# Performance work log

Measured on AMD Instinct MI355X. Metric: run time of the kernel, lower is better.

The kernel has to match this reference:

```python
import jax, jax.numpy as jnp
import numpy as np

A2B = 1.8897259886          # angstrom -> bohr
EV2HA = 0.0367493
NUM_RBF = 16
R_MIN = 0.5 * A2B
R_MAX = 4.0 * A2B           # r_max_angstroms=4.0 from gnn_config
RBF_WIDTH = (R_MAX - R_MIN) / NUM_RBF
N_NODES = 100_000
N_EDGES = 3_200_000
EMBED_DIM = 16
N_ELEMS = 4
CODES_PER_ELEM = 4          # all elements are core -> max_codes_per_element
TOTAL_CODES = N_ELEMS * CODES_PER_ELEM
NUM_PAIRS = 10
CODE_OWNER = np.repeat(np.arange(N_ELEMS), CODES_PER_ELEM)  # element owning each code


def setup_inputs() -> dict:
    key = jax.random.key(0)
    ks = jax.random.split(key, 12)
    N, E, D = N_NODES, N_EDGES, EMBED_DIM
    inv_sp = lambda v: np.float32(np.log(np.expm1(v)))  # inverse_softplus
    return {
        "elem_idx": jax.random.randint(ks[0], (N,), 0, N_ELEMS),
        "edge_index": jax.random.randint(ks[1], (2, E), 0, N),
        "distances": jax.random.uniform(ks[2], (E,), minval=1.0, maxval=7.5),  # bohr
        "pair_idx": jax.random.randint(ks[3], (E,), 0, NUM_PAIRS),
        "embed": jax.random.normal(ks[4], (N_ELEMS, D)),
        "fw1": jax.random.normal(ks[5], (D, NUM_RBF)) * 0.3,
        "fb1": jnp.zeros((D,)),
        "fw2": jax.random.normal(ks[6], (D, D)) * 0.3,
        "fb2": jnp.zeros((D,)),
        "mw1": jax.random.normal(ks[7], (D, D)) * 0.3,
        "mb1": jnp.zeros((D,)),
        "mw2": jax.random.normal(ks[8], (3, D)) * 0.05,  # zero-init in orig; small random for a live baseline
        "mb2": jnp.zeros((3,)),
        "codebook": jax.random.normal(ks[9], (TOTAL_CODES, D)),
        "raw_D_e": jnp.full((NUM_PAIRS,), inv_sp(0.1 * EV2HA)),
        "raw_alpha": jnp.full((NUM_PAIRS,), inv_sp(1.5 / A2B)),
        "raw_r0": jnp.full((NUM_PAIRS,), np.float32(3.0 * A2B)),
    }


def reference(elem_idx, edge_index, distances, pair_idx, embed,
              fw1, fb1, fw2, fb2, mw1, mb1, mw2, mb2,
              codebook, raw_D_e, raw_alpha, raw_r0):
    # --- EnvironmentEncoder: gather + edge filter + scatter_add ---
    h = embed[elem_idx]                                              # [N, D]
    centers = jnp.linspace(R_MIN, R_MAX, NUM_RBF, dtype=distances.dtype)
    rbf = jnp.exp(-0.5 * ((distances[:, None] - centers) / RBF_WIDTH) ** 2)  # [E, RBF]
    W = jax.nn.silu(rbf @ fw1.T + fb1) @ fw2.T + fb2                 # [E, D]
    src, tgt = edge_index[0], edge_index[1]
    messages = h[tgt] * W                                            # [E, D]
    agg = jax.ops.segment_sum(messages, src, num_segments=h.shape[0])
    h = h + agg                                                      # [N, D]

    # --- VectorQuantizer (eval path): per-element masked cdist + argmin ---
    d2 = (jnp.sum(h * h, axis=1, keepdims=True)
          - 2.0 * h @ codebook.T
          + jnp.sum(codebook * codebook, axis=1))                    # [N, C] squared dist
    owner = jnp.asarray(CODE_OWNER)
    valid = elem_idx[:, None] == owner[None, :]                      # [N, C]
    atom_types = jnp.argmin(jnp.where(valid, d2, jnp.inf), axis=1)   # [N]
    z_q = codebook[atom_types]                                       # [N, D]
    h_q = h + jax.lax.stop_gradient(z_q - h)                         # straight-through
    # all elements have >1 code -> commitment over all atoms
    vq_loss = 0.25 * jnp.mean((h - jax.lax.stop_gradient(z_q)) ** 2)

    # --- MorseParameterPredictor: edge gather + MLP ---
    pair_feat = h_q[src] + h_q[tgt]                                  # [E, D]
    delta = jax.nn.silu(pair_feat @ mw1.T + mb1) @ mw2.T + mb2       # [E, 3]

    D_e = jax.nn.softplus(raw_D_e[pair_idx] + delta[:, 0])
    alpha = jax.nn.softplus(raw_alpha[pair_idx] + delta[:, 1])
    r0 = raw_r0[pair_idx] + delta[:, 2]
    params = jnp.stack([D_e, alpha, r0], axis=-1)                    # [E, 3]
    return params, vq_loss
```

## Files before the change

kernel.cpp:

```cpp
#include <hip/hip_runtime.h>
#include <stdint.h>

#define A2B   1.8897259886f
#define R_MIN (0.5f * A2B)
#define R_MAX (4.0f * A2B)

#define EPB 2048

__global__ void __launch_bounds__(256) k_bucket(
        const int* __restrict__ src, const int* __restrict__ tgt,
        const int* __restrict__ elem, const float* __restrict__ dist,
        int* __restrict__ gCursor, float* __restrict__ dBuf,
        unsigned short* __restrict__ kBuf, int CAP, int SHIFT, int E)
{
    __shared__ int cnt[256], base_[256];
    int t = threadIdx.x;
    cnt[t] = 0;
    __syncthreads();
    int e0 = blockIdx.x * EPB;
    int eEnd = (e0 + EPB < E) ? e0 + EPB : E;

    float dv[8]; int bv[8]; unsigned short kv[8];
    #pragma unroll
    for (int j = 0; j < 8; ++j) {
        int e = e0 + t + j * 256;
        if (e < eEnd) {
            int s = src[e];
            int q = elem[tgt[e]];
            dv[j] = dist[e];
            int b = s >> SHIFT;
            bv[j] = b;
            kv[j] = (unsigned short)(((s - (b << SHIFT)) << 2) | q);
            atomicAdd(&cnt[b], 1);
        }
    }
    __syncthreads();
    if (cnt[t] > 0) base_[t] = atomicAdd(&gCursor[t], cnt[t]);
    __syncthreads();
    cnt[t] = 0;
    __syncthreads();
    #pragma unroll
    for (int j = 0; j < 8; ++j) {
        int e = e0 + t + j * 256;
        if (e < eEnd) {
            int b = bv[j];
            int pos = base_[b] + atomicAdd(&cnt[b], 1);
            if (pos < CAP) {
                size_t idx = (size_t)b * CAP + pos;
                dBuf[idx] = dv[j];
                kBuf[idx] = kv[j];
            }
        }
    }
}

__global__ void __launch_bounds__(256) k_bscan(
        const int* __restrict__ gCursor, int* __restrict__ bucketBase,
        int* __restrict__ offs4, int NBUK, int N4, int E)
{
    __shared__ int sd[256];
    int t = threadIdx.x;
    int v = (t < NBUK) ? gCursor[t] : 0;
    sd[t] = v; __syncthreads();
    #pragma unroll
    for (int o = 1; o < 256; o <<= 1) {
        int x = (t >= o) ? sd[t - o] : 0;
        __syncthreads();
        sd[t] += x;
        __syncthreads();
    }
    bucketBase[t] = sd[t] - v;
    if (t == 0) offs4[N4] = E;
}

__global__ void __launch_bounds__(256) k_bin(
        const float* __restrict__ dBuf, const unsigned short* __restrict__ kBuf,
        const int* __restrict__ gCursor, const int* __restrict__ bucketBase,
        int* __restrict__ offs4, float* __restrict__ payload,
        int CAP, int SHIFT, int N)
{
    __shared__ int lcnt[2048];
    __shared__ int sd[256];
    int t = threadIdx.x, b = blockIdx.x;
    int n0 = b << SHIFT;
    int n1 = n0 + (1 << SHIFT); if (n1 > N) n1 = N;
    int m  = (n1 - n0) * 4;
    int cntE = gCursor[b]; if (cntE > CAP) cntE = CAP;
    int base = bucketBase[b];
    for (int i = t; i < m; i += 256) lcnt[i] = 0;
    __syncthreads();
    const float* dB = dBuf + (size_t)b * CAP;
    const unsigned short* kB = kBuf + (size_t)b * CAP;
    for (int i = t; i < cntE; i += 256)
        atomicAdd(&lcnt[kB[i]], 1);
    __syncthreads();
    int v[8]; int tsum = 0; int b8 = t * 8;
    #pragma unroll
    for (int j = 0; j < 8; ++j) { v[j] = (b8 + j < m) ? lcnt[b8 + j] : 0; tsum += v[j]; }
    sd[t] = tsum; __syncthreads();
    #pragma unroll
    for (int o = 1; o < 256; o <<= 1) {
        int x = (t >= o) ? sd[t - o] : 0;
        __syncthreads();
        sd[t] += x;
        __syncthreads();
    }
    int run = sd[t] - tsum;
    #pragma unroll
    for (int j = 0; j < 8; ++j) {
        if (b8 + j < m) {
            int c = v[j];
            lcnt[b8 + j] = run;
            offs4[n0 * 4 + b8 + j] = base + run;
            run += c;
        }
    }
    __syncthreads();
    for (int i = t; i < cntE; i += 256) {
        int pos = atomicAdd(&lcnt[kB[i]], 1);
        payload[base + pos] = dB[i];
    }
}

__global__ void __launch_bounds__(256) k_gather(
        const int* __restrict__ elem, const float* __restrict__ embed,
        const float* __restrict__ codebook,
        const float* __restrict__ fw1, const float* __restrict__ fb1,
        const float* __restrict__ fw2, const float* __restrict__ fb2,
        const int* __restrict__ offs4, const float* __restrict__ payload,
        int* __restrict__ atype, float* __restrict__ loss, int N)
{
    __shared__ float4 s_fw1t[64];
    __shared__ float4 s_fw2v[64];
    __shared__ float s_cb[256];
    __shared__ float s_fb1[16], s_fb2[16], s_emb[64], s_cbn[16];
    __shared__ float s_red[4];
    int t = threadIdx.x;
    {
        float* f1 = (float*)s_fw1t;
        f1[(t & 15) * 16 + (t >> 4)] = fw1[t];
        float* f2 = (float*)s_fw2v;
        f2[t] = fw2[t];
        s_cb[t] = codebook[t];
    }
    if (t < 16) { s_fb1[t] = fb1[t]; s_fb2[t] = fb2[t]; }
    if (t < 64) s_emb[t] = embed[t];
    __syncthreads();
    if (t < 16) {
        float s = 0.f;
        #pragma unroll
        for (int j = 0; j < 16; ++j) { float c = s_cb[t * 16 + j]; s += c * c; }
        s_cbn[t] = s;
    }
    __syncthreads();

    int node = blockIdx.x * 32 + (t >> 3);
    int sub  = t & 7;
    float lp = 0.0f;
    float acc[16];
    #pragma unroll
    for (int j = 0; j < 16; ++j) acc[j] = 0.f;

    if (node < N) {
        const float invw   = 16.0f / (R_MAX - R_MIN);
        const float u0base = R_MIN * invw;
        const float kstep  = 16.0f / 15.0f;
        #pragma clang loop unroll(disable)
        for (int qq = 0; qq < 4; ++qq) {
            int b0 = offs4[node * 4 + qq], b1 = offs4[node * 4 + qq + 1];
            if (b0 == b1) continue;
            float G[16];
            #pragma unroll
            for (int j = 0; j < 16; ++j) G[j] = 0.f;
            for (int i = b0 + sub; i < b1; i += 16) {
                int ii = i + 8;
                bool has2 = (ii < b1);
                float d0 = payload[i];
                float d1 = has2 ? payload[ii] : d0;
                float ua = d0 * invw - u0base;
                float ub = d1 * invw - u0base;
                float g0[16], g1[16];
                #pragma unroll
                for (int i2 = 0; i2 < 16; ++i2) { g0[i2] = s_fb1[i2]; g1[i2] = s_fb1[i2]; }
                #pragma clang loop unroll(disable)
                for (int k = 0; k < 16; ++k) {
                    float r0 = __expf(-0.5f * ua * ua);
                    float r1 = __expf(-0.5f * ub * ub);
                    float4 w0 = s_fw1t[k*4+0], w1 = s_fw1t[k*4+1];
                    float4 w2 = s_fw1t[k*4+2], w3 = s_fw1t[k*4+3];
                    g0[0]+=r0*w0.x;  g0[1]+=r0*w0.y;  g0[2]+=r0*w0.z;  g0[3]+=r0*w0.w;
                    g0[4]+=r0*w1.x;  g0[5]+=r0*w1.y;  g0[6]+=r0*w1.z;  g0[7]+=r0*w1.w;
                    g0[8]+=r0*w2.x;  g0[9]+=r0*w2.y;  g0[10]+=r0*w2.z; g0[11]+=r0*w2.w;
                    g0[12]+=r0*w3.x; g0[13]+=r0*w3.y; g0[14]+=r0*w3.z; g0[15]+=r0*w3.w;
                    g1[0]+=r1*w0.x;  g1[1]+=r1*w0.y;  g1[2]+=r1*w0.z;  g1[3]+=r1*w0.w;
                    g1[4]+=r1*w1.x;  g1[5]+=r1*w1.y;  g1[6]+=r1*w1.z;  g1[7]+=r1*w1.w;
                    g1[8]+=r1*w2.x;  g1[9]+=r1*w2.y;  g1[10]+=r1*w2.z; g1[11]+=r1*w2.w;
                    g1[12]+=r1*w3.x; g1[13]+=r1*w3.y; g1[14]+=r1*w3.z; g1[15]+=r1*w3.w;
                    ua -= kstep; ub -= kstep;
                }
                #pragma unroll
                for (int i2 = 0; i2 < 16; ++i2) {
                    float a = g0[i2];
                    G[i2] += a * __builtin_amdgcn_rcpf(1.0f + __expf(-a));
                }
                if (has2) {
                    #pragma unroll
                    for (int i2 = 0; i2 < 16; ++i2) {
                        float a = g1[i2];
                        G[i2] += a * __builtin_amdgcn_rcpf(1.0f + __expf(-a));
                    }
                }
            }
            const float* er = s_emb + qq * 16;
            #pragma clang loop unroll_count(4)
            for (int j = 0; j < 16; ++j) {
                float4 f0 = s_fw2v[j*4+0], f1 = s_fw2v[j*4+1];
                float4 f2 = s_fw2v[j*4+2], f3 = s_fw2v[j*4+3];
                float w = G[0]*f0.x  + G[1]*f0.y  + G[2]*f0.z  + G[3]*f0.w
                        + G[4]*f1.x  + G[5]*f1.y  + G[6]*f1.z  + G[7]*f1.w
                        + G[8]*f2.x  + G[9]*f2.y  + G[10]*f2.z + G[11]*f2.w
                        + G[12]*f3.x + G[13]*f3.y + G[14]*f3.z + G[15]*f3.w;
                acc[j] += w * er[j];
            }
            if (sub == 0) {
                float nb = (float)(b1 - b0);
                #pragma unroll
                for (int j = 0; j < 16; ++j)
                    acc[j] += nb * s_fb2[j] * er[j];
            }
        }
        #pragma unroll
        for (int m = 1; m <= 4; m <<= 1) {
            #pragma unroll
            for (int j = 0; j < 16; ++j)
                acc[j] += __shfl_xor(acc[j], m, 64);
        }
        int qn = elem[node];
        float h[16], hh = 0.f;
        #pragma unroll
        for (int j = 0; j < 16; ++j) {
            h[j] = acc[j] + s_emb[qn * 16 + j];
            hh += h[j] * h[j];
        }
        float best = __builtin_inff(); int bi = 0;
        #pragma unroll
        for (int c = 0; c < 4; ++c) {
            int code = qn * 4 + c;
            float dot = 0.f;
            #pragma unroll
            for (int j = 0; j < 16; ++j) dot += h[j] * s_cb[code * 16 + j];
            float d2 = hh - 2.0f * dot + s_cbn[code];
            if (d2 < best) { best = d2; bi = code; }
        }
        if (sub == 0) {
            atype[node] = bi;
            #pragma unroll
            for (int j = 0; j < 16; ++j) {
                float df = h[j] - s_cb[bi * 16 + j];
                lp += df * df;
            }
        }
    }
    #pragma unroll
    for (int o = 32; o > 0; o >>= 1) lp += __shfl_down(lp, o, 64);
    int wid = t >> 6;
    if ((t & 63) == 0) s_red[wid] = lp;
    __syncthreads();
    if (t == 0) atomicAdd(loss, s_red[0] + s_red[1] + s_red[2] + s_red[3]);
}

__global__ void __launch_bounds__(256) k_table(
        const float* __restrict__ codebook,
        const float* __restrict__ mw1, const float* __restrict__ mb1,
        const float* __restrict__ mw2, const float* __restrict__ mb2,
        const float* __restrict__ rD, const float* __restrict__ rA,
        const float* __restrict__ rR,
        const float* __restrict__ loss, float4* __restrict__ table,
        float* __restrict__ out_loss, float inv_nd)
{
    __shared__ float s_cb[256], s_mw1[256], s_mb1[16], s_mw2[48], s_mb2[3];
    __shared__ float s_rd[10], s_ra[10], s_rr[10];
    int tid = threadIdx.x;
    s_cb[tid] = codebook[tid];
    s_mw1[tid] = mw1[tid];
    if (tid < 16) s_mb1[tid] = mb1[tid];
    if (tid < 48) s_mw2[tid] = mw2[tid];
    if (tid < 3)  s_mb2[tid] = mb2[tid];
    if (tid < 10) { s_rd[tid] = rD[tid]; s_ra[tid] = rA[tid]; s_rr[tid] = rR[tid]; }
    __syncthreads();

    int a = tid >> 4, b = tid & 15;
    float pf[16];
    #pragma unroll
    for (int j = 0; j < 16; ++j) pf[j] = s_cb[a * 16 + j] + s_cb[b * 16 + j];
    float hid[16];
    #pragma unroll
    for (int i = 0; i < 16; ++i) {
        float acc = s_mb1[i];
        #pragma unroll
        for (int j = 0; j < 16; ++j) acc += pf[j] * s_mw1[i * 16 + j];
        hid[i] = acc / (1.0f + __expf(-acc));
    }
    float del[3];
    #pragma unroll
    for (int r = 0; r < 3; ++r) {
        float acc = s_mb2[r];
        #pragma unroll
        for (int i = 0; i < 16; ++i) acc += hid[i] * s_mw2[r * 16 + i];
        del[r] = acc;
    }
    #pragma unroll
    for (int p = 0; p < 10; ++p) {
        float xd = s_rd[p] + del[0];
        float xa = s_ra[p] + del[1];
        float De = (xd > 20.f) ? xd : log1pf(__expf(xd));
        float al = (xa > 20.f) ? xa : log1pf(__expf(xa));
        float r0 = s_rr[p] + del[2];
        table[tid * 10 + p] = make_float4(De, al, r0, 0.f);
    }
    if (tid == 0) out_loss[0] = 0.25f * loss[0] * inv_nd;
}

__global__ void __launch_bounds__(256) k_out(
        const int* __restrict__ src, const int* __restrict__ tgt,
        const int* __restrict__ pidx, const int* __restrict__ atype,
        const float4* __restrict__ table, float2* __restrict__ out, int Ehalf)
{
    int i = blockIdx.x * 256 + threadIdx.x;
    if (i >= Ehalf) return;
    int2 s2 = ((const int2*)src)[i];
    int2 t2 = ((const int2*)tgt)[i];
    int2 p2 = ((const int2*)pidx)[i];
    int i0 = (atype[s2.x] * 16 + atype[t2.x]) * 10 + p2.x;
    int i1 = (atype[s2.y] * 16 + atype[t2.y]) * 10 + p2.y;
    float4 t0 = table[i0];
    float4 t1 = table[i1];
    float2* op = out + (size_t)3 * i;
    op[0] = make_float2(t0.x, t0.y);
    op[1] = make_float2(t0.z, t1.x);
    op[2] = make_float2(t1.y, t1.z);
}

extern "C" void kernel_launch(void* const* d_in, const int* in_sizes, int n_in,
                              void* d_out, int out_size, void* d_ws, size_t ws_size,
                              hipStream_t stream)
{
    (void)n_in;
    const int*   elem  = (const int*)d_in[0];
    const int*   eidx  = (const int*)d_in[1];
    const float* dist  = (const float*)d_in[2];
    const int*   pidx  = (const int*)d_in[3];
    const float* embed = (const float*)d_in[4];
    const float* fw1   = (const float*)d_in[5];
    const float* fb1   = (const float*)d_in[6];
    const float* fw2   = (const float*)d_in[7];
    const float* fb2   = (const float*)d_in[8];
    const float* mw1   = (const float*)d_in[9];
    const float* mb1   = (const float*)d_in[10];
    const float* mw2   = (const float*)d_in[11];
    const float* mb2   = (const float*)d_in[12];
    const float* cb    = (const float*)d_in[13];
    const float* rD    = (const float*)d_in[14];
    const float* rA    = (const float*)d_in[15];
    const float* rR    = (const float*)d_in[16];

    int N = in_sizes[0];
    int E = in_sizes[2];
    const int* src = eidx;
    const int* tgt = eidx + E;
    int N4 = N * 4;

    int SHIFT = 0;
    while ((1 << SHIFT) < (N + 255) / 256) SHIFT++;
    int NBUK = (N + (1 << SHIFT) - 1) >> SHIFT;
    long long expv = ((long long)E << SHIFT) / N;
    int CAP = (int)(expv + expv / 16 + 256);

    size_t outBytes = (size_t)out_size * 4;
    char* ob = (char*)d_out;
    size_t oc = 0;
    float* dBuf = (float*)(ob + oc);           oc += (size_t)NBUK * CAP * 4;
    unsigned short* kBuf = (unsigned short*)(ob + oc); oc += (size_t)NBUK * CAP * 2;
    oc = (oc + 3) & ~(size_t)3;
    float* payload = (float*)(ob + oc);        oc += (size_t)E * 4;
    int*   offs4   = (int*)(ob + oc);          oc += (size_t)(N4 + 1) * 4;
    if (oc > outBytes) return;

    char* ws = (char*)d_ws;
    size_t cur = 0;
    int*   gCursor    = (int*)(ws + cur);  cur += 256 * 4;
    float* loss       = (float*)(ws + cur); cur += 4;
    size_t clearB = cur;
    int*   bucketBase = (int*)(ws + cur);  cur += 256 * 4;
    int*   atype      = (int*)(ws + cur);  cur += (size_t)N * 4;
    cur = (cur + 15) & ~(size_t)15;
    float4* table     = (float4*)(ws + cur); cur += 2560 * sizeof(float4);
    if (ws_size < cur) return;

    hipMemsetAsync(d_ws, 0, clearB, stream);

    k_bucket<<<(E + EPB - 1) / EPB, 256, 0, stream>>>(
        src, tgt, elem, dist, gCursor, dBuf, kBuf, CAP, SHIFT, E);
    k_bscan<<<1, 256, 0, stream>>>(gCursor, bucketBase, offs4, NBUK, N4, E);
    k_bin<<<NBUK, 256, 0, stream>>>(dBuf, kBuf, gCursor, bucketBase,
                                    offs4, payload, CAP, SHIFT, N);
    k_gather<<<(N + 31) / 32, 256, 0, stream>>>(elem, embed, cb, fw1, fb1,
                                                fw2, fb2, offs4, payload,
                                                atype, loss, N);
    float* outl = (float*)d_out + (size_t)3 * E;
    k_table<<<1, 256, 0, stream>>>(cb, mw1, mb1, mw2, mb2, rD, rA, rR,
                                   loss, table, outl,
                                   1.0f / (float)((size_t)N * 16));
    k_out<<<(E / 2 + 255) / 256, 256, 0, stream>>>(src, tgt, pidx, atype, table,
                                                   (float2*)d_out, E / 2);
}
```

Baseline: 302.4 us.

## Bin edges per node only and pack source element into distance low bits

```diff
diff --git a/kernel.cpp b/kernel.cpp
--- a/kernel.cpp
+++ b/kernel.cpp
@@ -56,7 +56,7 @@
 
 __global__ void __launch_bounds__(256) k_bscan(
         const int* __restrict__ gCursor, int* __restrict__ bucketBase,
-        int* __restrict__ offs4, int NBUK, int N4, int E)
+        int* __restrict__ offs, int NBUK, int N, int E)
 {
     __shared__ int sd[256];
     int t = threadIdx.x;
@@ -70,21 +70,21 @@
         __syncthreads();
     }
     bucketBase[t] = sd[t] - v;
-    if (t == 0) offs4[N4] = E;
+    if (t == 0) offs[N] = E;
 }
 
 __global__ void __launch_bounds__(256) k_bin(
         const float* __restrict__ dBuf, const unsigned short* __restrict__ kBuf,
         const int* __restrict__ gCursor, const int* __restrict__ bucketBase,
-        int* __restrict__ offs4, float* __restrict__ payload,
+        int* __restrict__ offs, float* __restrict__ payload,
         int CAP, int SHIFT, int N)
 {
-    __shared__ int lcnt[2048];
+    __shared__ int lcnt[512];
     __shared__ int sd[256];
     int t = threadIdx.x, b = blockIdx.x;
     int n0 = b << SHIFT;
     int n1 = n0 + (1 << SHIFT); if (n1 > N) n1 = N;
-    int m  = (n1 - n0) * 4;
+    int m  = n1 - n0;
     int cntE = gCursor[b]; if (cntE > CAP) cntE = CAP;
     int base = bucketBase[b];
     for (int i = t; i < m; i += 256) lcnt[i] = 0;
@@ -92,11 +92,12 @@
     const float* dB = dBuf + (size_t)b * CAP;
     const unsigned short* kB = kBuf + (size_t)b * CAP;
     for (int i = t; i < cntE; i += 256)
-        atomicAdd(&lcnt[kB[i]], 1);
-    __syncthreads();
-    int v[8]; int tsum = 0; int b8 = t * 8;
-    #pragma unroll
-    for (int j = 0; j < 8; ++j) { v[j] = (b8 + j < m) ? lcnt[b8 + j] : 0; tsum += v[j]; }
+        atomicAdd(&lcnt[kB[i] >> 2], 1);
+    __syncthreads();
+    int b2 = t * 2;
+    int v0 = (b2 < m)     ? lcnt[b2]     : 0;
+    int v1 = (b2 + 1 < m) ? lcnt[b2 + 1] : 0;
+    int tsum = v0 + v1;
     sd[t] = tsum; __syncthreads();
     #pragma unroll
     for (int o = 1; o < 256; o <<= 1) {
@@ -106,19 +107,14 @@
         __syncthreads();
     }
     int run = sd[t] - tsum;
-    #pragma unroll
-    for (int j = 0; j < 8; ++j) {
-        if (b8 + j < m) {
-            int c = v[j];
-            lcnt[b8 + j] = run;
-            offs4[n0 * 4 + b8 + j] = base + run;
-            run += c;
-        }
-    }
+    if (b2 < m)     { lcnt[b2] = run;     offs[n0 + b2] = base + run;     run += v0; }
+    if (b2 + 1 < m) { lcnt[b2 + 1] = run; offs[n0 + b2 + 1] = base + run; run += v1; }
     __syncthreads();
     for (int i = t; i < cntE; i += 256) {
-        int pos = atomicAdd(&lcnt[kB[i]], 1);
-        payload[base + pos] = dB[i];
+        int kv = kB[i];
+        int pos = atomicAdd(&lcnt[kv >> 2], 1);
+        unsigned db = __float_as_uint(dB[i]);
+        payload[base + pos] = __uint_as_float((db & ~3u) | (unsigned)(kv & 3));
     }
 }
 
@@ -127,7 +123,7 @@
         const float* __restrict__ codebook,
         const float* __restrict__ fw1, const float* __restrict__ fb1,
         const float* __restrict__ fw2, const float* __restrict__ fb2,
-        const int* __restrict__ offs4, const float* __restrict__ payload,
+        const int* __restrict__ offs, const float* __restrict__ payload,
         int* __restrict__ atype, float* __restrict__ loss, int N)
 {
     __shared__ float4 s_fw1t[64];
@@ -154,86 +150,107 @@
     }
     __syncthreads();
 
-    int node = blockIdx.x * 32 + (t >> 3);
-    int sub  = t & 7;
+    int node = blockIdx.x * 64 + (t >> 2);
+    int sub  = t & 3;
     float lp = 0.0f;
-    float acc[16];
-    #pragma unroll
-    for (int j = 0; j < 16; ++j) acc[j] = 0.f;
-
     if (node < N) {
+        int o0 = offs[node], o1 = offs[node + 1];
+        float G0[16], G1[16], G2[16], G3[16];
+        #pragma unroll
+        for (int j = 0; j < 16; ++j) { G0[j]=0.f; G1[j]=0.f; G2[j]=0.f; G3[j]=0.f; }
+        float c0 = 0.f, c1 = 0.f, c2 = 0.f, c3 = 0.f;
+
         const float invw   = 16.0f / (R_MAX - R_MIN);
         const float u0base = R_MIN * invw;
         const float kstep  = 16.0f / 15.0f;
-        #pragma clang loop unroll(disable)
-        for (int qq = 0; qq < 4; ++qq) {
-            int b0 = offs4[node * 4 + qq], b1 = offs4[node * 4 + qq + 1];
-            if (b0 == b1) continue;
-            float G[16];
+        for (int i = o0 + sub; i < o1; i += 8) {
+            int ii = i + 4;
+            bool has2 = (ii < o1);
+            unsigned p0 = __float_as_uint(payload[i]);
+            unsigned p1 = has2 ? __float_as_uint(payload[ii]) : p0;
+            int q0 = (int)(p0 & 3u), q1 = (int)(p1 & 3u);
+            float d0 = __uint_as_float(p0 & ~3u);
+            float d1 = __uint_as_float(p1 & ~3u);
+            float ua = d0 * invw - u0base;
+            float ub = d1 * invw - u0base;
+            float g0[16], g1[16];
             #pragma unroll
-            for (int j = 0; j < 16; ++j) G[j] = 0.f;
-            for (int i = b0 + sub; i < b1; i += 16) {
-                int ii = i + 8;
-                bool has2 = (ii < b1);
-                float d0 = payload[i];
-                float d1 = has2 ? payload[ii] : d0;
-                float ua = d0 * invw - u0base;
-                float ub = d1 * invw - u0base;
-                float g0[16], g1[16];
-                #pragma unroll
-                for (int i2 = 0; i2 < 16; ++i2) { g0[i2] = s_fb1[i2]; g1[i2] = s_fb1[i2]; }
-                #pragma clang loop unroll(disable)
-                for (int k = 0; k < 16; ++k) {
-                    float r0 = __expf(-0.5f * ua * ua);
-                    float r1 = __expf(-0.5f * ub * ub);
-                    float4 w0 = s_fw1t[k*4+0], w1 = s_fw1t[k*4+1];
-                    float4 w2 = s_fw1t[k*4+2], w3 = s_fw1t[k*4+3];
-                    g0[0]+=r0*w0.x;  g0[1]+=r0*w0.y;  g0[2]+=r0*w0.z;  g0[3]+=r0*w0.w;
-                    g0[4]+=r0*w1.x;  g0[5]+=r0*w1.y;  g0[6]+=r0*w1.z;  g0[7]+=r0*w1.w;
-                    g0[8]+=r0*w2.x;  g0[9]+=r0*w2.y;  g0[10]+=r0*w2.z; g0[11]+=r0*w2.w;
-                    g0[12]+=r0*w3.x; g0[13]+=r0*w3.y; g0[14]+=r0*w3.z; g0[15]+=r0*w3.w;
-                    g1[0]+=r1*w0.x;  g1[1]+=r1*w0.y;  g1[2]+=r1*w0.z;  g1[3]+=r1*w0.w;
-                    g1[4]+=r1*w1.x;  g1[5]+=r1*w1.y;  g1[6]+=r1*w1.z;  g1[7]+=r1*w1.w;
-                    g1[8]+=r1*w2.x;  g1[9]+=r1*w2.y;  g1[10]+=r1*w2.z; g1[11]+=r1*w2.w;
-                    g1[12]+=r1*w3.x; g1[13]+=r1*w3.y; g1[14]+=r1*w3.z; g1[15]+=r1*w3.w;
-                    ua -= kstep; ub -= kstep;
-                }
+            for (int i2 = 0; i2 < 16; ++i2) { g0[i2] = s_fb1[i2]; g1[i2] = s_fb1[i2]; }
+            #pragma clang loop unroll(disable)
+            for (int k = 0; k < 16; ++k) {
+                float r0 = __expf(-0.5f * ua * ua);
+                float r1 = __expf(-0.5f * ub * ub);
+                float4 w0 = s_fw1t[k*4+0], w1 = s_fw1t[k*4+1];
+                float4 w2 = s_fw1t[k*4+2], w3 = s_fw1t[k*4+3];
+                g0[0]+=r0*w0.x;  g0[1]+=r0*w0.y;  g0[2]+=r0*w0.z;  g0[3]+=r0*w0.w;
+                g0[4]+=r0*w1.x;  g0[5]+=r0*w1.y;  g0[6]+=r0*w1.z;  g0[7]+=r0*w1.w;
+                g0[8]+=r0*w2.x;  g0[9]+=r0*w2.y;  g0[10]+=r0*w2.z; g0[11]+=r0*w2.w;
+                g0[12]+=r0*w3.x; g0[13]+=r0*w3.y; g0[14]+=r0*w3.z; g0[15]+=r0*w3.w;
+                g1[0]+=r1*w0.x;  g1[1]+=r1*w0.y;  g1[2]+=r1*w0.z;  g1[3]+=r1*w0.w;
+                g1[4]+=r1*w1.x;  g1[5]+=r1*w1.y;  g1[6]+=r1*w1.z;  g1[7]+=r1*w1.w;
+                g1[8]+=r1*w2.x;  g1[9]+=r1*w2.y;  g1[10]+=r1*w2.z; g1[11]+=r1*w2.w;
+                g1[12]+=r1*w3.x; g1[13]+=r1*w3.y; g1[14]+=r1*w3.z; g1[15]+=r1*w3.w;
+                ua -= kstep; ub -= kstep;
+            }
+            {
+                float m0 = (q0==0)?1.f:0.f, m1 = (q0==1)?1.f:0.f;
+                float m2 = (q0==2)?1.f:0.f, m3 = (q0==3)?1.f:0.f;
+                c0 += m0; c1 += m1; c2 += m2; c3 += m3;
                 #pragma unroll
                 for (int i2 = 0; i2 < 16; ++i2) {
                     float a = g0[i2];
-                    G[i2] += a * __builtin_amdgcn_rcpf(1.0f + __expf(-a));
+                    float s = a * __builtin_amdgcn_rcpf(1.0f + __expf(-a));
+                    G0[i2] += m0*s; G1[i2] += m1*s; G2[i2] += m2*s; G3[i2] += m3*s;
                 }
-                if (has2) {
-                    #pragma unroll
-                    for (int i2 = 0; i2 < 16; ++i2) {
-                        float a = g1[i2];
-                        G[i2] += a * __builtin_amdgcn_rcpf(1.0f + __expf(-a));
-                    }
+            }
+            if (has2) {
+                float m0 = (q1==0)?1.f:0.f, m1 = (q1==1)?1.f:0.f;
+                float m2 = (q1==2)?1.f:0.f, m3 = (q1==3)?1.f:0.f;
+                c0 += m0; c1 += m1; c2 += m2; c3 += m3;
+                #pragma unroll
+                for (int i2 = 0; i2 < 16; ++i2) {
+                    float a = g1[i2];
+                    float s = a * __builtin_amdgcn_rcpf(1.0f + __expf(-a));
+                    G0[i2] += m0*s; G1[i2] += m1*s; G2[i2] += m2*s; G3[i2] += m3*s;
                 }
             }
-            const float* er = s_emb + qq * 16;
-            #pragma clang loop unroll_count(4)
+        }
+        #pragma unroll
+        for (int mm = 1; mm <= 2; mm <<= 1) {
+            #pragma unroll
             for (int j = 0; j < 16; ++j) {
-                float4 f0 = s_fw2v[j*4+0], f1 = s_fw2v[j*4+1];
-                float4 f2 = s_fw2v[j*4+2], f3 = s_fw2v[j*4+3];
-                float w = G[0]*f0.x  + G[1]*f0.y  + G[2]*f0.z  + G[3]*f0.w
-                        + G[4]*f1.x  + G[5]*f1.y  + G[6]*f1.z  + G[7]*f1.w
-                        + G[8]*f2.x  + G[9]*f2.y  + G[10]*f2.z + G[11]*f2.w
-                        + G[12]*f3.x + G[13]*f3.y + G[14]*f3.z + G[15]*f3.w;
-                acc[j] += w * er[j];
-            }
-            if (sub == 0) {
-                float nb = (float)(b1 - b0);
-                #pragma unroll
-                for (int j = 0; j < 16; ++j)
-                    acc[j] += nb * s_fb2[j] * er[j];
-            }
-        }
-        #pragma unroll
-        for (int m = 1; m <= 4; m <<= 1) {
+                G0[j] += __shfl_xor(G0[j], mm, 64);
+                G1[j] += __shfl_xor(G1[j], mm, 64);
+                G2[j] += __shfl_xor(G2[j], mm, 64);
+                G3[j] += __shfl_xor(G3[j], mm, 64);
+            }
+            c0 += __shfl_xor(c0, mm, 64);
+            c1 += __shfl_xor(c1, mm, 64);
+            c2 += __shfl_xor(c2, mm, 64);
+            c3 += __shfl_xor(c3, mm, 64);
+        }
+        float Gs[16];
+        #pragma unroll
+        for (int j = 0; j < 16; ++j)
+            Gs[j] = (sub==0) ? G0[j] : (sub==1) ? G1[j] : (sub==2) ? G2[j] : G3[j];
+        float cs = (sub==0) ? c0 : (sub==1) ? c1 : (sub==2) ? c2 : c3;
+        const float* er = s_emb + sub * 16;
+        float acc[16];
+        #pragma clang loop unroll_count(4)
+        for (int j = 0; j < 16; ++j) {
+            float4 f0 = s_fw2v[j*4+0], f1 = s_fw2v[j*4+1];
+            float4 f2 = s_fw2v[j*4+2], f3 = s_fw2v[j*4+3];
+            float w = Gs[0]*f0.x  + Gs[1]*f0.y  + Gs[2]*f0.z  + Gs[3]*f0.w
+                    + Gs[4]*f1.x  + Gs[5]*f1.y  + Gs[6]*f1.z  + Gs[7]*f1.w
+                    + Gs[8]*f2.x  + Gs[9]*f2.y  + Gs[10]*f2.z + Gs[11]*f2.w
+                    + Gs[12]*f3.x + Gs[13]*f3.y + Gs[14]*f3.z + Gs[15]*f3.w;
+            acc[j] = (w + cs * s_fb2[j]) * er[j];
+        }
+        #pragma unroll
+        for (int mm = 1; mm <= 2; mm <<= 1) {
             #pragma unroll
             for (int j = 0; j < 16; ++j)
-                acc[j] += __shfl_xor(acc[j], m, 64);
+                acc[j] += __shfl_xor(acc[j], mm, 64);
         }
         int qn = elem[node];
         float h[16], hh = 0.f;
@@ -368,7 +385,6 @@
     int E = in_sizes[2];
     const int* src = eidx;
     const int* tgt = eidx + E;
-    int N4 = N * 4;
 
     int SHIFT = 0;
     while ((1 << SHIFT) < (N + 255) / 256) SHIFT++;
@@ -383,7 +399,7 @@
     unsigned short* kBuf = (unsigned short*)(ob + oc); oc += (size_t)NBUK * CAP * 2;
     oc = (oc + 3) & ~(size_t)3;
     float* payload = (float*)(ob + oc);        oc += (size_t)E * 4;
-    int*   offs4   = (int*)(ob + oc);          oc += (size_t)(N4 + 1) * 4;
+    int*   offs    = (int*)(ob + oc);          oc += (size_t)(N + 1) * 4;
     if (oc > outBytes) return;
 
     char* ws = (char*)d_ws;
@@ -401,11 +417,11 @@
 
     k_bucket<<<(E + EPB - 1) / EPB, 256, 0, stream>>>(
         src, tgt, elem, dist, gCursor, dBuf, kBuf, CAP, SHIFT, E);
-    k_bscan<<<1, 256, 0, stream>>>(gCursor, bucketBase, offs4, NBUK, N4, E);
+    k_bscan<<<1, 256, 0, stream>>>(gCursor, bucketBase, offs, NBUK, N, E);
     k_bin<<<NBUK, 256, 0, stream>>>(dBuf, kBuf, gCursor, bucketBase,
-                                    offs4, payload, CAP, SHIFT, N);
-    k_gather<<<(N + 31) / 32, 256, 0, stream>>>(elem, embed, cb, fw1, fb1,
-                                                fw2, fb2, offs4, payload,
+                                    offs, payload, CAP, SHIFT, N);
+    k_gather<<<(N + 63) / 64, 256, 0, stream>>>(elem, embed, cb, fw1, fb1,
+                                                fw2, fb2, offs, payload,
                                                 atype, loss, N);
     float* outl = (float*)d_out + (size_t)3 * E;
     k_table<<<1, 256, 0, stream>>>(cb, mw1, mb1, mw2, mb2, rD, rA, rR,
```

After: 259.7 us. -14.1%, faster.
